# Kernel tuning notes

Hardware: AMD Instinct MI355X
Metric: run time of the kernel (lower is better)

The kernel has to match this reference:

```python
import jax, jax.numpy as jnp
import numpy as np

N, IN_DIM, HEADS, OUT_DIM = 4096, 256, 4, 64

def setup_inputs() -> dict:
    key = jax.random.key(0)
    k1, k2, k3 = jax.random.split(key, 3)
    h = jax.random.normal(k1, (N, IN_DIM), dtype=jnp.float32)
    W = jax.random.normal(k2, (IN_DIM, HEADS * OUT_DIM), dtype=jnp.float32) * (1.0 / np.sqrt(IN_DIM))
    a = jax.random.normal(k3, (HEADS, 2 * OUT_DIM), dtype=jnp.float32) * 0.1
    return {"h": h, "W": W, "a": a}

def reference(h, W, a):
    # Wh: [N, heads, out_dim]
    Wh = (h @ W).reshape(N, HEADS, OUT_DIM)
    # Split additive attention vector a = [a_dst | a_src]; e[i,j,k] = lrelu(f_i[i,k] + f_j[j,k])
    # This is algebraically identical to LeakyReLU(((Wh_i||Wh_j) * a).sum(-1))
    f_i = jnp.einsum('nhd,hd->nh', Wh, a[:, :OUT_DIM])   # [N, heads]
    f_j = jnp.einsum('nhd,hd->nh', Wh, a[:, OUT_DIM:])   # [N, heads]
    e = jax.nn.leaky_relu(f_i[:, None, :] + f_j[None, :, :], negative_slope=0.2)  # [N,N,heads]
    attn = jax.nn.softmax(e, axis=1)  # softmax over source nodes j
    # dropout is identity in eval mode
    out = jnp.einsum('ijk,jkl->ikl', attn, Wh)  # [N, heads, out_dim]
    out = out.reshape(N, HEADS * OUT_DIM)       # concat=True
    return out, attn
```

## Files before the change

kernel.cpp:

```cpp
#include <hip/hip_runtime.h>
#include <math.h>

#define NN 4096
#define IN_DIM 256
#define HEADS 4
#define OUT_DIM 64

typedef float f32x4 __attribute__((ext_vector_type(4)));

__device__ __forceinline__ float fexp(float x){ return __expf(x); }

__global__ void k_gw(const float* __restrict__ h, const float* __restrict__ W,
                     const float* __restrict__ a,
                     float* __restrict__ Wh, float* __restrict__ fi, float* __restrict__ fjT,
                     float* __restrict__ E1j, float* __restrict__ E2j){
    __shared__ float4 hs4[16][64];
    const int i0 = blockIdx.x * 16;
    const int t  = threadIdx.x;
    const int w  = t >> 6, l = t & 63;
    {
        const float4* h4 = (const float4*)h;
        hs4[w][l]      = h4[(i0 + w) * 64 + l];
        hs4[w + 4][l]  = h4[(i0 + w + 4) * 64 + l];
        hs4[w + 8][l]  = h4[(i0 + w + 8) * 64 + l];
        hs4[w + 12][l] = h4[(i0 + w + 12) * 64 + l];
    }
    __syncthreads();
    const int r0 = w * 4;
    const float4* W4 = (const float4*)W;
    float4 acc[4];
    #pragma unroll
    for (int r = 0; r < 4; ++r) acc[r] = make_float4(0.f, 0.f, 0.f, 0.f);
    #pragma unroll 2
    for (int kq = 0; kq < 64; ++kq) {
        const float4 w0 = W4[(4 * kq + 0) * 64 + l];
        const float4 w1 = W4[(4 * kq + 1) * 64 + l];
        const float4 w2 = W4[(4 * kq + 2) * 64 + l];
        const float4 w3 = W4[(4 * kq + 3) * 64 + l];
        #pragma unroll
        for (int r = 0; r < 4; ++r) {
            const float4 hv = hs4[r0 + r][kq];
            acc[r].x = fmaf(hv.x, w0.x, acc[r].x);
            acc[r].y = fmaf(hv.x, w0.y, acc[r].y);
            acc[r].z = fmaf(hv.x, w0.z, acc[r].z);
            acc[r].w = fmaf(hv.x, w0.w, acc[r].w);
            acc[r].x = fmaf(hv.y, w1.x, acc[r].x);
            acc[r].y = fmaf(hv.y, w1.y, acc[r].y);
            acc[r].z = fmaf(hv.y, w1.z, acc[r].z);
            acc[r].w = fmaf(hv.y, w1.w, acc[r].w);
            acc[r].x = fmaf(hv.z, w2.x, acc[r].x);
            acc[r].y = fmaf(hv.z, w2.y, acc[r].y);
            acc[r].z = fmaf(hv.z, w2.z, acc[r].z);
            acc[r].w = fmaf(hv.z, w2.w, acc[r].w);
            acc[r].x = fmaf(hv.w, w3.x, acc[r].x);
            acc[r].y = fmaf(hv.w, w3.y, acc[r].y);
            acc[r].z = fmaf(hv.w, w3.z, acc[r].z);
            acc[r].w = fmaf(hv.w, w3.w, acc[r].w);
        }
    }
    const int head = l >> 4;
    const int g = l & 15;
    const float4 a4D = ((const float4*)a)[head * 32 + g];
    const float4 a4S = ((const float4*)a)[head * 32 + 16 + g];
    #pragma unroll
    for (int r = 0; r < 4; ++r) {
        const int n = i0 + r0 + r;
        ((float4*)Wh)[n * 64 + l] = acc[r];
        float p1 = acc[r].x * a4D.x + acc[r].y * a4D.y + acc[r].z * a4D.z + acc[r].w * a4D.w;
        float p2 = acc[r].x * a4S.x + acc[r].y * a4S.y + acc[r].z * a4S.z + acc[r].w * a4S.w;
        #pragma unroll
        for (int off = 8; off; off >>= 1) {
            p1 += __shfl_down(p1, off);
            p2 += __shfl_down(p2, off);
        }
        if (g == 0) {
            fi[n * 4 + head]   = p1;
            fjT[head * NN + n] = p2;
            E1j[n * 4 + head]  = fexp(p2);
            E2j[n * 4 + head]  = fexp(0.2f * p2);
        }
    }
}

__global__ void k_rp(const float* __restrict__ fjT, const float* __restrict__ Wh,
                     float* __restrict__ fs, float* __restrict__ Whp){
    const int j0 = blockIdx.x * 8;
    const int t = threadIdx.x;
    const int hh = t >> 6, d = t & 63;
    const int base = hh * NN;
    float v[8]; int cnt[8];
    #pragma unroll
    for (int r = 0; r < 8; ++r) { v[r] = fjT[base + j0 + r]; cnt[r] = 0; }
    #pragma unroll 4
    for (int m = 0; m < 64; ++m) {
        const int jp = d + m * 64;
        const float x = fjT[base + jp];
        #pragma unroll
        for (int r = 0; r < 8; ++r)
            cnt[r] += (x < v[r] || (x == v[r] && jp < (j0 + r))) ? 1 : 0;
    }
    #pragma unroll
    for (int r = 0; r < 8; ++r) {
        int c = cnt[r];
        #pragma unroll
        for (int off = 32; off; off >>= 1) c += __shfl_down(c, off);
        const int rank = __shfl(c, 0);
        if (d == 0) fs[base + rank] = v[r];
        Whp[(size_t)(base + rank) * 64 + d] = Wh[(j0 + r) * 256 + hh * 64 + d];
    }
}

__global__ void k_chunks(const float* __restrict__ fs, const float* __restrict__ Whp,
                         float* __restrict__ r1, float* __restrict__ r2x,
                         float* __restrict__ rz1, float* __restrict__ rz2x,
                         float* __restrict__ cs1, float* __restrict__ cs2,
                         float* __restrict__ cz1, float* __restrict__ cz2){
    const int b = blockIdx.x;
    const int H = b >> 6, c = b & 63;
    const int t = threadIdx.x;
    const int w = t >> 6, d = t & 63;
    const int base = H * NN;
    const int qw = c * 64 + w * 16;
    float wv[16], e1s[16], e2s[16];
    #pragma unroll
    for (int s = 0; s < 16; ++s) {
        const int q = qw + s;
        const float f = fs[base + q];
        e1s[s] = fexp(f);
        e2s[s] = fexp(0.2f * f);
        wv[s]  = Whp[(size_t)(base + q) * 64 + d];
    }
    float p2[16], s1[16], lz1[16], lz2[16];
    float acc2 = 0.f, z2 = 0.f;
    #pragma unroll
    for (int s = 0; s < 16; ++s) {
        p2[s] = acc2; lz2[s] = z2;
        acc2 += e2s[s] * wv[s]; z2 += e2s[s];
    }
    float acc1 = 0.f, z1 = 0.f;
    #pragma unroll
    for (int s = 15; s >= 0; --s) {
        acc1 += e1s[s] * wv[s]; z1 += e1s[s];
        s1[s] = acc1; lz1[s] = z1;
    }
    __shared__ float t1[4][64], t2[4][64], tz1[4], tz2[4];
    t1[w][d] = acc1; t2[w][d] = acc2;
    if (d == 0) { tz1[w] = z1; tz2[w] = z2; }
    __syncthreads();
    float off1 = 0.f, off2 = 0.f, zo1 = 0.f, zo2 = 0.f;
    #pragma unroll
    for (int w2 = 0; w2 < 4; ++w2) {
        if (w2 > w) { off1 += t1[w2][d]; zo1 += tz1[w2]; }
        if (w2 < w) { off2 += t2[w2][d]; zo2 += tz2[w2]; }
    }
    #pragma unroll
    for (int s = 0; s < 16; ++s) {
        const int q = qw + s;
        r1 [(size_t)(base + q) * 64 + d] = off1 + s1[s];
        r2x[(size_t)(base + q) * 64 + d] = off2 + p2[s];
        if (d == 0) {
            rz1 [base + q] = zo1 + lz1[s];
            rz2x[base + q] = zo2 + lz2[s];
        }
    }
    if (w == 0) {
        cs1[b * 64 + d] = off1 + acc1;
        if (d == 0) cz1[b] = zo1 + z1;
    }
    if (w == 3) {
        cs2[b * 64 + d] = off2 + acc2;
        if (d == 0) cz2[b] = zo2 + z2;
    }
}

__global__ void k_scan(const float* __restrict__ cs1, const float* __restrict__ cs2,
                       const float* __restrict__ cz1, const float* __restrict__ cz2,
                       float* __restrict__ S1, float* __restrict__ S2,
                       float* __restrict__ Z1, float* __restrict__ Z2){
    const int H = blockIdx.x;
    const int t = threadIdx.x;
    if (t < 64) {
        const int d = t; float acc = 0.f;
        S1[(H * 65 + 64) * 64 + d] = 0.f;
        #pragma unroll 8
        for (int c = 63; c >= 0; --c) { acc += cs1[(H * 64 + c) * 64 + d]; S1[(H * 65 + c) * 64 + d] = acc; }
    } else if (t < 128) {
        const int d = t - 64; float acc = 0.f;
        S2[(H * 65 + 0) * 64 + d] = 0.f;
        #pragma unroll 8
        for (int c = 0; c < 64; ++c) { acc += cs2[(H * 64 + c) * 64 + d]; S2[(H * 65 + c + 1) * 64 + d] = acc; }
    } else if (t == 128) {
        float acc = 0.f; Z1[H * 65 + 64] = 0.f;
        for (int c = 63; c >= 0; --c) { acc += cz1[H * 64 + c]; Z1[H * 65 + c] = acc; }
    } else if (t == 129) {
        float acc = 0.f; Z2[H * 65 + 0] = 0.f;
        for (int c = 0; c < 64; ++c) { acc += cz2[H * 64 + c]; Z2[H * 65 + c + 1] = acc; }
    }
}

__global__ void k_qa(const float* __restrict__ fi, const float* __restrict__ fs,
                     const float* __restrict__ r1, const float* __restrict__ r2x,
                     const float* __restrict__ rz1, const float* __restrict__ rz2x,
                     const float* __restrict__ S1, const float* __restrict__ S2,
                     const float* __restrict__ Z1, const float* __restrict__ Z2,
                     const f32x4* __restrict__ E1j4, const f32x4* __restrict__ E2j4,
                     float* __restrict__ out, f32x4* __restrict__ attn){
    const int i = blockIdx.x;
    const int t = threadIdx.x;
    const int hh = t >> 6, d = t & 63;
    const int base = hh * NN;
    __shared__ float sth[4], sa1[4], sa2[4];

    const float s = fi[i * 4 + hh];
    const float thr = -s;
    const unsigned long long m1 = __ballot(fs[base + d * 64] < thr);
    const int k1 = __popcll(m1);
    int p = 0;
    if (k1 > 0) {
        const int cc = k1 - 1;
        const unsigned long long m2 = __ballot(fs[base + cc * 64 + d] < thr);
        p = cc * 64 + __popcll(m2);
    }
    float a1, a2, z1, z2;
    if (p == NN) {
        a1 = 0.f; z1 = 0.f;
        a2 = S2[(hh * 65 + 64) * 64 + d]; z2 = Z2[hh * 65 + 64];
    } else {
        const int c = p >> 6;
        a1 = r1 [(size_t)(base + p) * 64 + d] + S1[(hh * 65 + c + 1) * 64 + d];
        z1 = rz1[base + p]                    + Z1[hh * 65 + c + 1];
        a2 = r2x[(size_t)(base + p) * 64 + d] + S2[(hh * 65 + c) * 64 + d];
        z2 = rz2x[base + p]                   + Z2[hh * 65 + c];
    }
    const float E1 = fexp(s), E2 = fexp(0.2f * s);
    const float iz = 1.f / (E1 * z1 + E2 * z2);
    __builtin_nontemporal_store((E1 * a1 + E2 * a2) * iz, &out[i * 256 + t]);
    if (d == 0) {
        sth[hh] = fexp(thr);
        sa1[hh] = E1 * iz;
        sa2[hh] = E2 * iz;
    }
    __syncthreads();
    const float th0 = sth[0], th1 = sth[1], th2 = sth[2], th3 = sth[3];
    const float c10 = sa1[0], c11 = sa1[1], c12 = sa1[2], c13 = sa1[3];
    const float c20 = sa2[0], c21 = sa2[1], c22 = sa2[2], c23 = sa2[3];
    f32x4* __restrict__ row = attn + (size_t)i * NN;
    #pragma unroll
    for (int it = 0; it < 16; ++it) {
        const int j = it * 256 + t;
        const f32x4 e1 = E1j4[j];
        const f32x4 e2 = E2j4[j];
        f32x4 o;
        o.x = (e1.x >= th0) ? c10 * e1.x : c20 * e2.x;
        o.y = (e1.y >= th1) ? c11 * e1.y : c21 * e2.y;
        o.z = (e1.z >= th2) ? c12 * e1.z : c22 * e2.z;
        o.w = (e1.w >= th3) ? c13 * e1.w : c23 * e2.w;
        __builtin_nontemporal_store(o, &row[j]);
    }
}

extern "C" void kernel_launch(void* const* d_in, const int* in_sizes, int n_in,
                              void* d_out, int out_size, void* d_ws, size_t ws_size,
                              hipStream_t stream) {
    const float* h = (const float*)d_in[0];
    const float* W = (const float*)d_in[1];
    const float* a = (const float*)d_in[2];
    float* out = (float*)d_out;
    float* ws  = (float*)d_ws;

    float* Wh   = ws;
    float* Whp  = Wh   + 1048576;
    float* fi   = Whp  + 1048576;
    float* fjT  = fi   + 16384;
    float* E1j  = fjT  + 16384;
    float* E2j  = E1j  + 16384;
    float* fs   = E2j  + 16384;
    float* cs1  = fs   + 16384;
    float* cs2  = cs1  + 16384;
    float* cz1  = cs2  + 16384;
    float* cz2  = cz1  + 256;
    float* S1   = cz2  + 256;
    float* S2   = S1   + 16640;
    float* Z1   = S2   + 16640;
    float* Z2   = Z1   + 260;
    float* r1   = Z2   + 260;
    float* r2x  = r1   + 1048576;
    float* rz1  = r2x  + 1048576;
    float* rz2x = rz1  + 16384;

    k_gw    <<<NN / 16, 256, 0, stream>>>(h, W, a, Wh, fi, fjT, E1j, E2j);
    k_rp    <<<NN / 8, 256, 0, stream>>>(fjT, Wh, fs, Whp);
    k_chunks<<<HEADS * 64, 256, 0, stream>>>(fs, Whp, r1, r2x, rz1, rz2x, cs1, cs2, cz1, cz2);
    k_scan  <<<HEADS, 256, 0, stream>>>(cs1, cs2, cz1, cz2, S1, S2, Z1, Z2);

    float* attn = out + (NN * HEADS * OUT_DIM);
    k_qa    <<<NN, 256, 0, stream>>>(fi, fs, r1, r2x, rz1, rz2x, S1, S2, Z1, Z2,
                                     (const f32x4*)E1j, (const f32x4*)E2j,
                                     out, (f32x4*)attn);
}
```

Baseline: 133.4 us.

## Split attention write into separate kernel tiling rows to reuse shared E vectors

```diff
diff --git a/kernel.cpp b/kernel.cpp
--- a/kernel.cpp
+++ b/kernel.cpp
@@ -198,19 +198,17 @@
     }
 }
 
-__global__ void k_qa(const float* __restrict__ fi, const float* __restrict__ fs,
-                     const float* __restrict__ r1, const float* __restrict__ r2x,
-                     const float* __restrict__ rz1, const float* __restrict__ rz2x,
-                     const float* __restrict__ S1, const float* __restrict__ S2,
-                     const float* __restrict__ Z1, const float* __restrict__ Z2,
-                     const f32x4* __restrict__ E1j4, const f32x4* __restrict__ E2j4,
-                     float* __restrict__ out, f32x4* __restrict__ attn){
+__global__ void k_q(const float* __restrict__ fi, const float* __restrict__ fs,
+                    const float* __restrict__ r1, const float* __restrict__ r2x,
+                    const float* __restrict__ rz1, const float* __restrict__ rz2x,
+                    const float* __restrict__ S1, const float* __restrict__ S2,
+                    const float* __restrict__ Z1, const float* __restrict__ Z2,
+                    float* __restrict__ out, float* __restrict__ thrE,
+                    float* __restrict__ A1, float* __restrict__ A2){
     const int i = blockIdx.x;
     const int t = threadIdx.x;
     const int hh = t >> 6, d = t & 63;
     const int base = hh * NN;
-    __shared__ float sth[4], sa1[4], sa2[4];
-
     const float s = fi[i * 4 + hh];
     const float thr = -s;
     const unsigned long long m1 = __ballot(fs[base + d * 64] < thr);
@@ -236,26 +234,46 @@
     const float iz = 1.f / (E1 * z1 + E2 * z2);
     __builtin_nontemporal_store((E1 * a1 + E2 * a2) * iz, &out[i * 256 + t]);
     if (d == 0) {
-        sth[hh] = fexp(thr);
-        sa1[hh] = E1 * iz;
-        sa2[hh] = E2 * iz;
+        thrE[i * 4 + hh] = fexp(thr);
+        A1[i * 4 + hh]   = E1 * iz;
+        A2[i * 4 + hh]   = E2 * iz;
+    }
+}
+
+__global__ void k_attn(const f32x4* __restrict__ E1j4, const f32x4* __restrict__ E2j4,
+                       const f32x4* __restrict__ thrE4, const f32x4* __restrict__ A14,
+                       const f32x4* __restrict__ A24, f32x4* __restrict__ attn){
+    __shared__ f32x4 se1[1024], se2[1024];
+    const int b = blockIdx.x;
+    const int jt = b & 3;
+    const int i0 = (b >> 2) * 16;
+    const int t = threadIdx.x;
+    const int jbase = jt * 1024;
+    #pragma unroll
+    for (int u = 0; u < 4; ++u) {
+        const int q = u * 256 + t;
+        se1[q] = E1j4[jbase + q];
+        se2[q] = E2j4[jbase + q];
     }
     __syncthreads();
-    const float th0 = sth[0], th1 = sth[1], th2 = sth[2], th3 = sth[3];
-    const float c10 = sa1[0], c11 = sa1[1], c12 = sa1[2], c13 = sa1[3];
-    const float c20 = sa2[0], c21 = sa2[1], c22 = sa2[2], c23 = sa2[3];
-    f32x4* __restrict__ row = attn + (size_t)i * NN;
-    #pragma unroll
-    for (int it = 0; it < 16; ++it) {
-        const int j = it * 256 + t;
-        const f32x4 e1 = E1j4[j];
-        const f32x4 e2 = E2j4[j];
-        f32x4 o;
-        o.x = (e1.x >= th0) ? c10 * e1.x : c20 * e2.x;
-        o.y = (e1.y >= th1) ? c11 * e1.y : c21 * e2.y;
-        o.z = (e1.z >= th2) ? c12 * e1.z : c22 * e2.z;
-        o.w = (e1.w >= th3) ? c13 * e1.w : c23 * e2.w;
-        __builtin_nontemporal_store(o, &row[j]);
+    for (int ii = 0; ii < 16; ++ii) {
+        const int i = i0 + ii;
+        const f32x4 th = thrE4[i];
+        const f32x4 c1 = A14[i];
+        const f32x4 c2 = A24[i];
+        f32x4* __restrict__ row = attn + (size_t)i * NN + jbase;
+        #pragma unroll
+        for (int u = 0; u < 4; ++u) {
+            const int q = u * 256 + t;
+            const f32x4 e1 = se1[q];
+            const f32x4 e2 = se2[q];
+            f32x4 o;
+            o.x = (e1.x >= th.x) ? c1.x * e1.x : c2.x * e2.x;
+            o.y = (e1.y >= th.y) ? c1.y * e1.y : c2.y * e2.y;
+            o.z = (e1.z >= th.z) ? c1.z * e1.z : c2.z * e2.z;
+            o.w = (e1.w >= th.w) ? c1.w * e1.w : c2.w * e2.w;
+            __builtin_nontemporal_store(o, &row[q]);
+        }
     }
 }
 
@@ -287,14 +305,19 @@
     float* r2x  = r1   + 1048576;
     float* rz1  = r2x  + 1048576;
     float* rz2x = rz1  + 16384;
+    float* thrE = rz2x + 16384;
+    float* A1   = thrE + 16384;
+    float* A2   = A1   + 16384;
 
     k_gw    <<<NN / 16, 256, 0, stream>>>(h, W, a, Wh, fi, fjT, E1j, E2j);
     k_rp    <<<NN / 8, 256, 0, stream>>>(fjT, Wh, fs, Whp);
     k_chunks<<<HEADS * 64, 256, 0, stream>>>(fs, Whp, r1, r2x, rz1, rz2x, cs1, cs2, cz1, cz2);
     k_scan  <<<HEADS, 256, 0, stream>>>(cs1, cs2, cz1, cz2, S1, S2, Z1, Z2);
+    k_q     <<<NN, 256, 0, stream>>>(fi, fs, r1, r2x, rz1, rz2x, S1, S2, Z1, Z2,
+                                     out, thrE, A1, A2);
 
     float* attn = out + (NN * HEADS * OUT_DIM);
-    k_qa    <<<NN, 256, 0, stream>>>(fi, fs, r1, r2x, rz1, rz2x, S1, S2, Z1, Z2,
-                                     (const f32x4*)E1j, (const f32x4*)E2j,
-                                     out, (f32x4*)attn);
-}
+    k_attn  <<<1024, 256, 0, stream>>>((const f32x4*)E1j, (const f32x4*)E2j,
+                                       (const f32x4*)thrE, (const f32x4*)A1,
+                                       (const f32x4*)A2, (f32x4*)attn);
+}
```

Measured after the change: 138.2 us. +3.6%, slower.
